# Kernel tuning notes

Hardware: AMD Instinct MI355X
Metric: run time of the kernel (lower is better)

## Reference

```python
import jax, jax.numpy as jnp
import numpy as np

K = 7
PAD = K // 2
BN_EPS = 1e-5


def _unfold(x):
    # x: (B, C, H, W) -> (B, C, K*K, H, W), torch.F.unfold row-major kernel order
    B, C, H, W = x.shape
    xp = jnp.pad(x, ((0, 0), (0, 0), (PAD, PAD), (PAD, PAD)))
    patches = [xp[:, :, i:i + H, j:j + W] for i in range(K) for j in range(K)]
    return jnp.stack(patches, axis=2)


def setup_inputs() -> dict:
    key = jax.random.key(0)
    ks = jax.random.split(key, 6)
    B, C, H, W = 1, 256, 80, 80
    Cp = 19
    return {
        "x": jax.random.normal(ks[0], (B, C, H, W), jnp.float32),
        "coarse_probs": jax.random.uniform(ks[1], (B, Cp, H, W), jnp.float32),
        "sigma": jnp.ones((1,), jnp.float32),
        "w_feat": jax.random.normal(ks[2], (C, C), jnp.float32) * 0.05,
        "w_fuse": jax.random.normal(ks[3], (C, C), jnp.float32) * 0.05,
        "bn_gamma": jnp.ones((C,), jnp.float32),
        "bn_beta": jnp.zeros((C,), jnp.float32),
        "bn_mean": jax.random.normal(ks[4], (C,), jnp.float32) * 0.1,
        "bn_var": jax.random.uniform(ks[5], (C,), jnp.float32) + 0.5,
    }


def reference(x, coarse_probs, sigma, w_feat, w_fuse, bn_gamma, bn_beta, bn_mean, bn_var):
    # BatchNorm2d (inference, running stats)
    inv = jax.lax.rsqrt(bn_var + BN_EPS)
    xn = (x - bn_mean[None, :, None, None]) * (inv * bn_gamma)[None, :, None, None] \
         + bn_beta[None, :, None, None]

    # affinity from coarse probs over K*K neighborhood
    up = _unfold(coarse_probs)                      # (B, Cp, K2, H, W)
    center = up[:, :, (K * K - 1) // 2][:, :, None]  # (B, Cp, 1, H, W)
    dist_sq = jnp.sum((up - center) ** 2, axis=1)    # (B, K2, H, W)
    denom = 2.0 * jax.nn.relu(sigma[0]) ** 2 + 1e-8
    affinity = jax.nn.softmax(jnp.exp(-dist_sq / denom), axis=1)

    # feature_conv (1x1, no bias), unfold, weighted aggregation
    messages = jnp.einsum('oc,bchw->bohw', w_feat, xn)
    um = _unfold(messages)                           # (B, C, K2, H, W)
    agg = jnp.sum(um * affinity[:, None], axis=2)    # (B, C, H, W)

    refined = jnp.einsum('oc,bchw->bohw', w_fuse, agg)
    return x + refined
```

## Files before the change

### kernel.cpp

```cpp
#include <hip/hip_runtime.h>
#include <math.h>

#define HW_ 6400
#define C_ 256
#define CP_ 19

__global__ __launch_bounds__(256) void wgemm_kernel(
    const float* __restrict__ wfeat, const float* __restrict__ wfuse,
    const float* __restrict__ g, const float* __restrict__ be,
    const float* __restrict__ mu, const float* __restrict__ var,
    float* __restrict__ WT, float* __restrict__ wsum)
{
    const int o = blockIdx.x, c = threadIdx.x;
    __shared__ float row[C_];
    __shared__ float red[C_];
    row[c] = wfuse[o * C_ + c];
    __syncthreads();
    float acc = 0.0f;
#pragma unroll 8
    for (int m = 0; m < C_; ++m) acc += row[m] * wfeat[m * C_ + c];
    float scale = g[c] * rsqrtf(var[c] + 1e-5f);
    float shift = be[c] - mu[c] * scale;
    WT[c * C_ + o] = acc * scale;
    red[c] = acc * shift;
    __syncthreads();
    for (int s = 128; s > 0; s >>= 1) {
        if (c < s) red[c] += red[c + s];
        __syncthreads();
    }
    if (c == 0) wsum[o] = red[0];
}

__global__ __launch_bounds__(256) void affinity_kernel(
    const float* __restrict__ cp, const float* __restrict__ sigma,
    float* __restrict__ aff, float* __restrict__ S)
{
    const int lane = threadIdx.x & 63;
    const int p = blockIdx.x * 4 + (threadIdx.x >> 6);
    const int h = p / 80, w = p - h * 80;
    const int k = (lane < 49) ? lane : 48;
    const int i = k / 7, j = k - i * 7;
    const int hh = h + i - 3, ww = w + j - 3;
    const bool ok = (hh >= 0) & (hh < 80) & (ww >= 0) & (ww < 80);
    const float msk = ok ? 1.0f : 0.0f;
    int q = hh * 80 + ww;
    q = min(max(q, 0), HW_ - 1);

    float s = fmaxf(sigma[0], 0.0f);
    float inv_denom = 1.0f / (2.0f * s * s + 1e-8f);

    float d = 0.0f;
#pragma unroll
    for (int c = 0; c < CP_; ++c) {
        float u = cp[c * HW_ + q];
        float ctr = __shfl(u, 24, 64);
        float t = u * msk - ctr;
        d += t * t;
    }
    float raw = __expf(-d * inv_denom);
    float e = (lane < 49) ? __expf(raw) : 0.0f;
    float einb = (ok && lane < 49) ? e : 0.0f;
    float sum = e, sumi = einb;
#pragma unroll
    for (int off = 32; off; off >>= 1) {
        sum  += __shfl_xor(sum,  off, 64);
        sumi += __shfl_xor(sumi, off, 64);
    }
    if (lane < 49) aff[k * HW_ + p] = e / sum;
    if (lane == 0) S[p] = sumi / sum;
}

__global__ __launch_bounds__(256) void aggx_kernel(
    const float* __restrict__ x, const float* __restrict__ aff,
    float* __restrict__ agg)
{
    int task = blockIdx.x * 256 + threadIdx.x;
    int c = task / 1600;
    int r = task - c * 1600;
    int h = r / 20;
    int w0 = (r - h * 20) * 4;
    int p0 = h * 80 + w0;
    const float* m = x + c * HW_;
    float acc[4] = {0.0f, 0.0f, 0.0f, 0.0f};
#pragma unroll
    for (int i = 0; i < 7; ++i) {
        int hh = h + i - 3;
        if (hh < 0 || hh >= 80) continue;
        const float* mrow = m + hh * 80;
        float mv[10];
#pragma unroll
        for (int t = 0; t < 10; ++t) {
            int ww = w0 - 3 + t;
            mv[t] = (ww >= 0 && ww < 80) ? mrow[ww] : 0.0f;
        }
#pragma unroll
        for (int j = 0; j < 7; ++j) {
            float a[4];
            *(float4*)a = *(const float4*)&aff[(i * 7 + j) * HW_ + p0];
            acc[0] += a[0] * mv[j];
            acc[1] += a[1] * mv[j + 1];
            acc[2] += a[2] * mv[j + 2];
            acc[3] += a[3] * mv[j + 3];
        }
    }
    *(float4*)&agg[c * HW_ + p0] = *(float4*)acc;
}

__global__ __launch_bounds__(256) void gemm_kernel(
    const float* __restrict__ AT, const float* __restrict__ B,
    const float* __restrict__ wsum, const float* __restrict__ S,
    const float* __restrict__ resid, float* __restrict__ C,
    int M, int N, int K)
{
    __shared__ float sA[16][64];
    __shared__ float sB[16][64];
    const int bm = blockIdx.y * 64, bn = blockIdx.x * 64;
    const int tx = threadIdx.x & 15, ty = threadIdx.x >> 4;
    const int e = threadIdx.x * 4;
    const int ka = e >> 6, ra = e & 63;
    float acc[4][4] = {};
    for (int k0 = 0; k0 < K; k0 += 16) {
        *(float4*)&sA[ka][ra] = *(const float4*)&AT[(k0 + ka) * M + bm + ra];
        *(float4*)&sB[ka][ra] = *(const float4*)&B[(k0 + ka) * N + bn + ra];
        __syncthreads();
#pragma unroll
        for (int kk = 0; kk < 16; ++kk) {
            float a[4], b[4];
            *(float4*)a = *(const float4*)&sA[kk][ty * 4];
            *(float4*)b = *(const float4*)&sB[kk][tx * 4];
#pragma unroll
            for (int i = 0; i < 4; ++i)
#pragma unroll
                for (int j = 0; j < 4; ++j) acc[i][j] += a[i] * b[j];
        }
        __syncthreads();
    }
    float s4[4];
    *(float4*)s4 = *(const float4*)&S[bn + tx * 4];
#pragma unroll
    for (int i = 0; i < 4; ++i) {
        int row = bm + ty * 4 + i;
        int off = row * N + bn + tx * 4;
        float ws = wsum[row];
        float x4[4];
        *(float4*)x4 = *(const float4*)&resid[off];
        float r[4];
#pragma unroll
        for (int j = 0; j < 4; ++j) r[j] = acc[i][j] + ws * s4[j] + x4[j];
        *(float4*)&C[off] = *(float4*)r;
    }
}

extern "C" void kernel_launch(void* const* d_in, const int* in_sizes, int n_in,
                              void* d_out, int out_size, void* d_ws, size_t ws_size,
                              hipStream_t stream) {
    const float* x      = (const float*)d_in[0];
    const float* cp     = (const float*)d_in[1];
    const float* sigma  = (const float*)d_in[2];
    const float* w_feat = (const float*)d_in[3];
    const float* w_fuse = (const float*)d_in[4];
    const float* g      = (const float*)d_in[5];
    const float* be     = (const float*)d_in[6];
    const float* mu     = (const float*)d_in[7];
    const float* var    = (const float*)d_in[8];
    float* out = (float*)d_out;

    float* ws_f = (float*)d_ws;
    float* WT   = ws_f;
    float* wsum = WT + 65536;
    float* aff  = wsum + 256;
    float* S    = aff + 313600;
    float* aggx = S + 6400;

    wgemm_kernel<<<256, 256, 0, stream>>>(w_feat, w_fuse, g, be, mu, var, WT, wsum);
    affinity_kernel<<<1600, 256, 0, stream>>>(cp, sigma, aff, S);
    aggx_kernel<<<1600, 256, 0, stream>>>(x, aff, aggx);
    gemm_kernel<<<dim3(100, 4), 256, 0, stream>>>(WT, aggx, wsum, S, x, out, C_, HW_, C_);
}
```

Before: 151.4 us.

## Use bf16 MFMA for fused-weight GEMM with transposed bf16 aggregation output

Replaces the fp32 SIMT tiled GEMM with a bf16 MFMA 16x16x32 GEMM. The aggregation kernel is restructured to hold the 49 affinity weights per pixel in registers, stage x rows in shared memory per channel, and write a pixel-major bf16 transposed layout. The composed weight matrix is also stored in bf16. The aim is to cut GEMM compute time and aggregation memory traffic, at the cost of bf16 precision loss and a much smaller grid (100 blocks for the GEMM, 400 for aggregation).

```diff
diff --git a/kernel.cpp b/kernel.cpp
--- a/kernel.cpp
+++ b/kernel.cpp
@@ -4,12 +4,22 @@
 #define HW_ 6400
 #define C_ 256
 #define CP_ 19
+#define CH_ 16
+
+typedef __bf16 bf16x8 __attribute__((ext_vector_type(8)));
+typedef float  f32x4  __attribute__((ext_vector_type(4)));
+
+static __device__ __forceinline__ unsigned short f2bf(float f) {
+    union { float f; unsigned int u; } x; x.f = f;
+    unsigned int r = x.u + 0x7FFF + ((x.u >> 16) & 1);
+    return (unsigned short)(r >> 16);
+}
 
 __global__ __launch_bounds__(256) void wgemm_kernel(
     const float* __restrict__ wfeat, const float* __restrict__ wfuse,
     const float* __restrict__ g, const float* __restrict__ be,
     const float* __restrict__ mu, const float* __restrict__ var,
-    float* __restrict__ WT, float* __restrict__ wsum)
+    unsigned short* __restrict__ WTb, float* __restrict__ wsum)
 {
     const int o = blockIdx.x, c = threadIdx.x;
     __shared__ float row[C_];
@@ -21,7 +31,7 @@
     for (int m = 0; m < C_; ++m) acc += row[m] * wfeat[m * C_ + c];
     float scale = g[c] * rsqrtf(var[c] + 1e-5f);
     float shift = be[c] - mu[c] * scale;
-    WT[c * C_ + o] = acc * scale;
+    WTb[o * C_ + c] = f2bf(acc * scale);
     red[c] = acc * shift;
     __syncthreads();
     for (int s = 128; s > 0; s >>= 1) {
@@ -70,84 +80,105 @@
     if (lane == 0) S[p] = sumi / sum;
 }
 
-__global__ __launch_bounds__(256) void aggx_kernel(
+__global__ __launch_bounds__(256) void aggT_kernel(
     const float* __restrict__ x, const float* __restrict__ aff,
-    float* __restrict__ agg)
-{
-    int task = blockIdx.x * 256 + threadIdx.x;
-    int c = task / 1600;
-    int r = task - c * 1600;
-    int h = r / 20;
-    int w0 = (r - h * 20) * 4;
-    int p0 = h * 80 + w0;
-    const float* m = x + c * HW_;
-    float acc[4] = {0.0f, 0.0f, 0.0f, 0.0f};
-#pragma unroll
-    for (int i = 0; i < 7; ++i) {
-        int hh = h + i - 3;
-        if (hh < 0 || hh >= 80) continue;
-        const float* mrow = m + hh * 80;
-        float mv[10];
-#pragma unroll
-        for (int t = 0; t < 10; ++t) {
-            int ww = w0 - 3 + t;
-            mv[t] = (ww >= 0 && ww < 80) ? mrow[ww] : 0.0f;
+    unsigned short* __restrict__ aggT)
+{
+    const int p = blockIdx.x * 256 + threadIdx.x;
+    const int h = p / 80, w = p - h * 80;
+    const int c0 = blockIdx.y * CH_;
+
+    float a[49];
+#pragma unroll
+    for (int k = 0; k < 49; ++k) a[k] = aff[k * HW_ + p];
+
+    const int h0 = (blockIdx.x * 256) / 80;
+    const int h1 = (blockIdx.x * 256 + 255) / 80;
+    const int rlo = max(h0 - 3, 0);
+    const int rhi = min(h1 + 3, 79);
+    const int nel = (rhi - rlo + 1) * 80;
+
+    __shared__ float xs[800];
+    float obuf[8];
+
+    for (int cc = 0; cc < CH_; ++cc) {
+        const int c = c0 + cc;
+        const float* xc = x + c * HW_ + rlo * 80;
+        for (int t = threadIdx.x; t < nel; t += 256) xs[t] = xc[t];
+        __syncthreads();
+        float acc = 0.0f;
+#pragma unroll
+        for (int i = 0; i < 7; ++i) {
+            int hh = h + i - 3;
+            if (hh >= 0 && hh < 80) {
+                int rbase = (hh - rlo) * 80 + w - 3;
+#pragma unroll
+                for (int j = 0; j < 7; ++j) {
+                    int ww = w + j - 3;
+                    float v = (ww >= 0 && ww < 80) ? xs[rbase + j] : 0.0f;
+                    acc += a[i * 7 + j] * v;
+                }
+            }
         }
-#pragma unroll
-        for (int j = 0; j < 7; ++j) {
-            float a[4];
-            *(float4*)a = *(const float4*)&aff[(i * 7 + j) * HW_ + p0];
-            acc[0] += a[0] * mv[j];
-            acc[1] += a[1] * mv[j + 1];
-            acc[2] += a[2] * mv[j + 2];
-            acc[3] += a[3] * mv[j + 3];
-        }
-    }
-    *(float4*)&agg[c * HW_ + p0] = *(float4*)acc;
-}
-
-__global__ __launch_bounds__(256) void gemm_kernel(
-    const float* __restrict__ AT, const float* __restrict__ B,
-    const float* __restrict__ wsum, const float* __restrict__ S,
-    const float* __restrict__ resid, float* __restrict__ C,
-    int M, int N, int K)
-{
-    __shared__ float sA[16][64];
-    __shared__ float sB[16][64];
-    const int bm = blockIdx.y * 64, bn = blockIdx.x * 64;
-    const int tx = threadIdx.x & 15, ty = threadIdx.x >> 4;
-    const int e = threadIdx.x * 4;
-    const int ka = e >> 6, ra = e & 63;
-    float acc[4][4] = {};
-    for (int k0 = 0; k0 < K; k0 += 16) {
-        *(float4*)&sA[ka][ra] = *(const float4*)&AT[(k0 + ka) * M + bm + ra];
-        *(float4*)&sB[ka][ra] = *(const float4*)&B[(k0 + ka) * N + bn + ra];
-        __syncthreads();
-#pragma unroll
-        for (int kk = 0; kk < 16; ++kk) {
-            float a[4], b[4];
-            *(float4*)a = *(const float4*)&sA[kk][ty * 4];
-            *(float4*)b = *(const float4*)&sB[kk][tx * 4];
-#pragma unroll
-            for (int i = 0; i < 4; ++i)
-#pragma unroll
-                for (int j = 0; j < 4; ++j) acc[i][j] += a[i] * b[j];
+        obuf[cc & 7] = acc;
+        if ((cc & 7) == 7) {
+            unsigned int pk[4];
+#pragma unroll
+            for (int t = 0; t < 4; ++t)
+                pk[t] = (unsigned int)f2bf(obuf[2 * t]) |
+                        ((unsigned int)f2bf(obuf[2 * t + 1]) << 16);
+            *(uint4*)&aggT[p * C_ + c0 + (cc & ~7)] =
+                make_uint4(pk[0], pk[1], pk[2], pk[3]);
         }
         __syncthreads();
     }
-    float s4[4];
-    *(float4*)s4 = *(const float4*)&S[bn + tx * 4];
-#pragma unroll
-    for (int i = 0; i < 4; ++i) {
-        int row = bm + ty * 4 + i;
-        int off = row * N + bn + tx * 4;
-        float ws = wsum[row];
-        float x4[4];
-        *(float4*)x4 = *(const float4*)&resid[off];
-        float r[4];
-#pragma unroll
-        for (int j = 0; j < 4; ++j) r[j] = acc[i][j] + ws * s4[j] + x4[j];
-        *(float4*)&C[off] = *(float4*)r;
+}
+
+__global__ __launch_bounds__(256) void mfma_gemm_kernel(
+    const unsigned short* __restrict__ WTb, const unsigned short* __restrict__ aggT,
+    const float* __restrict__ wsum, const float* __restrict__ S,
+    const float* __restrict__ x, float* __restrict__ out)
+{
+    const int wave = threadIdx.x >> 6, lane = threadIdx.x & 63;
+    const int q = lane >> 4, l15 = lane & 15;
+    const int bm = blockIdx.y * 64;
+    const int n0 = blockIdx.x * 256 + wave * 64;
+
+    f32x4 acc[4][4];
+#pragma unroll
+    for (int mi = 0; mi < 4; ++mi)
+#pragma unroll
+        for (int ni = 0; ni < 4; ++ni) acc[mi][ni] = (f32x4){0.f, 0.f, 0.f, 0.f};
+
+#pragma unroll
+    for (int k0 = 0; k0 < 256; k0 += 32) {
+        bf16x8 af[4], bf[4];
+#pragma unroll
+        for (int mi = 0; mi < 4; ++mi)
+            af[mi] = *(const bf16x8*)&WTb[(bm + mi * 16 + l15) * C_ + k0 + q * 8];
+#pragma unroll
+        for (int ni = 0; ni < 4; ++ni)
+            bf[ni] = *(const bf16x8*)&aggT[(n0 + ni * 16 + l15) * C_ + k0 + q * 8];
+#pragma unroll
+        for (int mi = 0; mi < 4; ++mi)
+#pragma unroll
+            for (int ni = 0; ni < 4; ++ni)
+                acc[mi][ni] = __builtin_amdgcn_mfma_f32_16x16x32_bf16(
+                    af[mi], bf[ni], acc[mi][ni], 0, 0, 0);
+    }
+
+#pragma unroll
+    for (int mi = 0; mi < 4; ++mi) {
+#pragma unroll
+        for (int ni = 0; ni < 4; ++ni) {
+            int p = n0 + ni * 16 + l15;
+            float Sp = S[p];
+#pragma unroll
+            for (int r = 0; r < 4; ++r) {
+                int m = bm + mi * 16 + q * 4 + r;
+                out[m * HW_ + p] = x[m * HW_ + p] + wsum[m] * Sp + acc[mi][ni][r];
+            }
+        }
     }
 }
 
@@ -165,15 +196,15 @@
     const float* var    = (const float*)d_in[8];
     float* out = (float*)d_out;
 
-    float* ws_f = (float*)d_ws;
-    float* WT   = ws_f;
-    float* wsum = WT + 65536;
-    float* aff  = wsum + 256;
-    float* S    = aff + 313600;
-    float* aggx = S + 6400;
-
-    wgemm_kernel<<<256, 256, 0, stream>>>(w_feat, w_fuse, g, be, mu, var, WT, wsum);
+    char* wsb = (char*)d_ws;
+    unsigned short* WTb  = (unsigned short*)wsb;
+    unsigned short* aggT = (unsigned short*)(wsb + 131072);
+    float* wsum = (float*)(wsb + 131072 + 3276800);
+    float* S    = wsum + 256;
+    float* aff  = S + HW_;
+
+    wgemm_kernel<<<256, 256, 0, stream>>>(w_feat, w_fuse, g, be, mu, var, WTb, wsum);
     affinity_kernel<<<1600, 256, 0, stream>>>(cp, sigma, aff, S);
-    aggx_kernel<<<1600, 256, 0, stream>>>(x, aff, aggx);
-    gemm_kernel<<<dim3(100, 4), 256, 0, stream>>>(WT, aggx, wsum, S, x, out, C_, HW_, C_);
-}
+    aggT_kernel<<<dim3(25, 16), 256, 0, stream>>>(x, aff, aggT);
+    mfma_gemm_kernel<<<dim3(25, 4), 256, 0, stream>>>(WTb, aggT, wsum, S, x, out);
+}
```

After: 152.9 us. No clear change (+1.0%).
